# Kernel optimization log

Hardware: AMD Instinct MI355X
Metric: run time of the kernel (lower is better)

## Reference

```python
import jax, jax.numpy as jnp
import numpy as np

B, S, D = 4, 2048, 512      # batch, seq_len, input_dim
E, H = 512, 8               # embed_dim, n_heads
HD = E // H                 # head_dim
ALPHA = 1.0                 # LRSA temperature


def setup_inputs() -> dict:
    key = jax.random.key(0)
    kx, kw1, kw2 = jax.random.split(key, 3)
    # xavier_uniform bounds for the two Linear layers (bias init is 0, as in module)
    b_qkv = float(np.sqrt(6.0 / (D + 3 * E)))
    b_o = float(np.sqrt(6.0 / (E + E)))
    return {
        "x": jax.random.normal(kx, (B, S, D), dtype=jnp.float32),
        "Wqkv": jax.random.uniform(kw1, (3 * E, D), jnp.float32, -b_qkv, b_qkv),
        "bqkv": jnp.zeros((3 * E,), jnp.float32),
        "Wo": jax.random.uniform(kw2, (E, E), jnp.float32, -b_o, b_o),
        "bo": jnp.zeros((E,), jnp.float32),
    }


def reference(x, Wqkv, bqkv, Wo, bo):
    Bx, Sx, _ = x.shape
    # QKV projection: [B,S,3E] -> [B,S,H,3*HD] -> [B,H,S,3*HD]
    qkv = (x @ Wqkv.T + bqkv).reshape(Bx, Sx, H, 3 * HD).transpose(0, 2, 1, 3)
    q, k, v = jnp.split(qkv, 3, axis=-1)  # each [B,H,S,HD]

    # LRSA: pairwise squared L2 distance logits ||q_i - k_j||^2
    q_norm2 = jnp.sum(q * q, axis=-1, keepdims=True)        # [B,H,S,1]
    k_norm2 = jnp.sum(k * k, axis=-1)[..., None, :]         # [B,H,1,S]
    qk = jnp.einsum("bhqd,bhkd->bhqk", q, k)                # [B,H,S,S]
    logits = q_norm2 - 2.0 * qk + k_norm2

    # global normalizers: frobenius norm of q, max per-token L2 norm of x
    fro_q = jnp.sqrt(jnp.sum(q * q))
    inf_2_x = jnp.max(jnp.sqrt(jnp.sum(x * x, axis=-1)))
    logits = logits / fro_q / inf_2_x

    attention = jax.nn.softmax(-ALPHA * logits, axis=-1)    # [B,H,S,S]
    values = jnp.einsum("bhqk,bhkd->bhqd", attention, v)    # [B,H,S,HD]
    values = values.transpose(0, 2, 1, 3).reshape(Bx, Sx, E)
    return values @ Wo.T + bo
```

## Files before the change

kernel.cpp:

```cpp
#include <hip/hip_runtime.h>
#include <hip/hip_bf16.h>
#include <math.h>

#define B_ 4
#define S_ 2048
#define D_ 512
#define E_ 512
#define H_ 8
#define HD_ 64
#define ALPHA_ 1.0f
#define M_ (B_*S_)
#define LOG2E_ 1.44269504088896340736f

typedef __attribute__((ext_vector_type(8))) short bf16x8;
typedef __attribute__((ext_vector_type(4))) float f32x4;
typedef __attribute__((ext_vector_type(16))) float f32x16;

__device__ inline unsigned short f2bf(float f) {
    union { __hip_bfloat16 h; unsigned short u; } cv;
    cv.h = __float2bfloat16(f);
    return cv.u;
}
__device__ inline unsigned pack2bf(float a, float b) {
    union { __hip_bfloat162 h; unsigned u; } cv;
    cv.h = __float22bfloat162_rn(make_float2(a, b));
    return cv.u;
}
__device__ inline void gload16(const void* g, void* l) {
    __builtin_amdgcn_global_load_lds(
        (const __attribute__((address_space(1))) unsigned int*)g,
        (__attribute__((address_space(3))) unsigned int*)l, 16, 0, 0);
}
__device__ inline void gload4(const void* g, void* l) {
    __builtin_amdgcn_global_load_lds(
        (const __attribute__((address_space(1))) unsigned int*)g,
        (__attribute__((address_space(3))) unsigned int*)l, 4, 0, 0);
}

__global__ __launch_bounds__(256) void prep(const float* __restrict__ x,
                                            const float* __restrict__ Wqkv,
                                            const float* __restrict__ Wo,
                                            unsigned short* __restrict__ xbf,
                                            unsigned short* __restrict__ Wqkvb,
                                            unsigned short* __restrict__ Wob,
                                            float* __restrict__ xmax) {
    const int t   = threadIdx.x;
    const int bid = blockIdx.x;
    if (bid < 2048) {
        __shared__ float red[4];
        const int wid = t >> 6, lane = t & 63;
        const int row = bid * 4 + wid;
        const float* xr = &x[(size_t)row * D_ + lane * 8];
        const float4 a = *(const float4*)xr;
        const float4 b = *(const float4*)(xr + 4);
        float ss = a.x*a.x + a.y*a.y + a.z*a.z + a.w*a.w
                 + b.x*b.x + b.y*b.y + b.z*b.z + b.w*b.w;
        uint4 o;
        o.x = pack2bf(a.x, a.y); o.y = pack2bf(a.z, a.w);
        o.z = pack2bf(b.x, b.y); o.w = pack2bf(b.z, b.w);
        *(uint4*)&xbf[(size_t)row * D_ + lane * 8] = o;
        #pragma unroll
        for (int off = 32; off; off >>= 1) ss += __shfl_xor(ss, off);
        if (lane == 0) red[wid] = ss;
        __syncthreads();
        if (t == 0)
            xmax[bid] = fmaxf(fmaxf(red[0], red[1]), fmaxf(red[2], red[3]));
    } else {
        const int i  = (bid - 2048) * 256 + t;
        const int nq = 3 * E_ * D_ / 8;
        const float* src; unsigned short* dst; int j;
        if (i < nq) { src = Wqkv; dst = Wqkvb; j = i; }
        else        { src = Wo;   dst = Wob;   j = i - nq; }
        const float4 a = *(const float4*)&src[(size_t)j * 8];
        const float4 b = *(const float4*)&src[(size_t)j * 8 + 4];
        uint4 o;
        o.x = pack2bf(a.x, a.y); o.y = pack2bf(a.z, a.w);
        o.z = pack2bf(b.x, b.y); o.w = pack2bf(b.z, b.w);
        *(uint4*)&dst[(size_t)j * 8] = o;
    }
}

template<int N, int MODE>
__global__ __launch_bounds__(256) void gemm_mfma(const unsigned short* __restrict__ Abf,
                                                 const unsigned short* __restrict__ Wbf,
                                                 const float* __restrict__ bias,
                                                 void* __restrict__ out0,
                                                 void* __restrict__ out1,
                                                 void* __restrict__ out2,
                                                 float* __restrict__ part,
                                                 float* __restrict__ kn2) {
    __shared__ __align__(16) char At[16384];
    __shared__ __align__(16) char Wt[16384];

    const int t  = threadIdx.x;
    const int w  = t >> 6;
    const int l  = t & 63;
    const int g  = l >> 4;
    const int c  = l & 15;
    const int wm = w >> 1;
    const int wn = w & 1;
    const int m0 = blockIdx.y * 128;
    const int n0 = blockIdx.x * 128;

    f32x4 acc[4][4];
    #pragma unroll
    for (int i = 0; i < 4; ++i)
        #pragma unroll
        for (int j = 0; j < 4; ++j)
            #pragma unroll
            for (int r = 0; r < 4; ++r) acc[i][j][r] = 0.f;

    const int lr3 = l >> 3;
    const int colSwz = ((l & 7) * 16) ^ (lr3 << 4);
    const char* pA = (const char*)Abf + (size_t)(m0 + w * 8 + lr3) * 1024 + colSwz;
    const char* pB = (const char*)Wbf + (size_t)(n0 + w * 8 + lr3) * 1024 + colSwz;
    char* lA = At + w * 1024;
    char* lB = Wt + w * 1024;

    for (int k0 = 0; k0 < 512; k0 += 64) {
        __syncthreads();
        #pragma unroll
        for (int j = 0; j < 4; ++j) {
            gload16(pA + (size_t)j * 32768 + k0 * 2, lA + j * 4096);
            gload16(pB + (size_t)j * 32768 + k0 * 2, lB + j * 4096);
        }
        __syncthreads();

        bf16x8 af[4][2], wf[4][2];
        #pragma unroll
        for (int mt = 0; mt < 4; ++mt) {
            const int row = wm * 64 + mt * 16 + c;
            const int sw  = (row & 7) << 4;
            #pragma unroll
            for (int kc = 0; kc < 2; ++kc)
                af[mt][kc] = *(const bf16x8*)(At + row * 128 + (((kc * 4 + g) * 16) ^ sw));
        }
        #pragma unroll
        for (int nt = 0; nt < 4; ++nt) {
            const int row = wn * 64 + nt * 16 + c;
            const int sw  = (row & 7) << 4;
            #pragma unroll
            for (int kc = 0; kc < 2; ++kc)
                wf[nt][kc] = *(const bf16x8*)(Wt + row * 128 + (((kc * 4 + g) * 16) ^ sw));
        }
        #pragma unroll
        for (int mt = 0; mt < 4; ++mt)
            #pragma unroll
            for (int nt = 0; nt < 4; ++nt) {
                acc[mt][nt] = __builtin_amdgcn_mfma_f32_16x16x32_bf16(af[mt][0], wf[nt][0], acc[mt][nt], 0, 0, 0);
                acc[mt][nt] = __builtin_amdgcn_mfma_f32_16x16x32_bf16(af[mt][1], wf[nt][1], acc[mt][nt], 0, 0, 0);
            }
    }

    if (MODE == 1) {
        #pragma unroll
        for (int mt = 0; mt < 4; ++mt)
            #pragma unroll
            for (int reg = 0; reg < 4; ++reg) {
                const int m = m0 + wm * 64 + mt * 16 + g * 4 + reg;
                #pragma unroll
                for (int nt = 0; nt < 4; ++nt) {
                    const int n = n0 + wn * 64 + nt * 16 + c;
                    ((float*)out0)[(size_t)m * N + n] = acc[mt][nt][reg] + bias[n];
                }
            }
        return;
    }

    const int hb  = 2 * blockIdx.x + wn;
    const int cls = hb % 3;
    const int h   = hb / 3;
    const int b   = m0 >> 11;
    const int s0w = (m0 & 2047) + wm * 64;
    const size_t bhS = ((size_t)b * H_ + h) * S_;

    float kp[4][4];
    #pragma unroll
    for (int i = 0; i < 4; ++i)
        #pragma unroll
        for (int j = 0; j < 4; ++j) kp[i][j] = 0.f;

    if (cls == 2) {
        unsigned short* Vt_ = (unsigned short*)out2;
        #pragma unroll
        for (int nt = 0; nt < 4; ++nt) {
            const int n = n0 + wn * 64 + nt * 16 + c;
            const float bv = bias[n];
            const int d = nt * 16 + c;
            unsigned short* dbase = Vt_ + (((size_t)b * H_ + h) * HD_ + d) * S_ + s0w;
            #pragma unroll
            for (int mt = 0; mt < 4; ++mt) {
                uint2 pk;
                pk.x = pack2bf(acc[mt][nt][0] + bv, acc[mt][nt][1] + bv);
                pk.y = pack2bf(acc[mt][nt][2] + bv, acc[mt][nt][3] + bv);
                *(uint2*)&dbase[mt * 16 + g * 4] = pk;
            }
        }
    } else {
        unsigned short* dst0 = (cls == 0) ? (unsigned short*)out0 : (unsigned short*)out1;
        #pragma unroll
        for (int nt = 0; nt < 4; ++nt) {
            const int n = n0 + wn * 64 + nt * 16 + c;
            const float bv = bias[n];
            const int d = nt * 16 + c;
            #pragma unroll
            for (int mt = 0; mt < 4; ++mt)
                #pragma unroll
                for (int reg = 0; reg < 4; ++reg) {
                    const int s = s0w + mt * 16 + g * 4 + reg;
                    const float val = acc[mt][nt][reg] + bv;
                    kp[mt][reg] = fmaf(val, val, kp[mt][reg]);
                    dst0[(bhS + s) * HD_ + d] = f2bf(val);
                }
        }
    }

    __syncthreads();
    if (cls == 1) {
        float* scratch = (float*)At + wm * 1088;
        #pragma unroll
        for (int i = 0; i < 16; ++i) scratch[l * 17 + i] = kp[i >> 2][i & 3];
        asm volatile("s_waitcnt lgkmcnt(0)" ::: "memory");
        __builtin_amdgcn_sched_barrier(0);
        float sum = 0.f;
        #pragma unroll
        for (int cc = 0; cc < 16; ++cc)
            sum += scratch[(g * 16 + cc) * 17 + c];
        const int s = s0w + (c >> 2) * 16 + g * 4 + (c & 3);
        kn2[bhS + s] = sum;
    }
    __syncthreads();

    float qss = 0.f;
    if (cls == 0) {
        #pragma unroll
        for (int i = 0; i < 4; ++i)
            #pragma unroll
            for (int j = 0; j < 4; ++j) qss += kp[i][j];
    }
    float* red = (float*)At;
    red[t] = qss;
    __syncthreads();
    for (int s = 128; s; s >>= 1) {
        if (t < s) red[t] += red[t + s];
        __syncthreads();
    }
    if (t == 0) part[blockIdx.y * gridDim.x + blockIdx.x] = red[0];
}

__global__ __launch_bounds__(256) void finalize_scale(const float* __restrict__ part,
                                                      const float* __restrict__ xmax,
                                                      float* __restrict__ scal) {
    __shared__ float rs[256], rm[256];
    const int t = threadIdx.x;
    float ss = 0.f, mx = 0.f;
    for (int i = t; i < 768; i += 256) ss += part[i];
    for (int i = t; i < 2048; i += 256) mx = fmaxf(mx, xmax[i]);
    rs[t] = ss; rm[t] = mx;
    __syncthreads();
    for (int s = 128; s; s >>= 1) {
        if (t < s) { rs[t] += rs[t + s]; rm[t] = fmaxf(rm[t], rm[t + s]); }
        __syncthreads();
    }
    if (t == 0) scal[0] = ALPHA_ * LOG2E_ / (sqrtf(rs[0]) * sqrtf(rm[0]));
}

__global__ __launch_bounds__(256, 2) void attn_mfma(const unsigned short* __restrict__ Qb,
                                                    const unsigned short* __restrict__ Kb,
                                                    const unsigned short* __restrict__ Vtb,
                                                    const float* __restrict__ KN2,
                                                    const float* __restrict__ scal,
                                                    unsigned short* __restrict__ VALS) {
    __shared__ __align__(16) char lds[33280];
    char* Kl  = lds;
    char* Vl  = lds + 16384;
    char* knl = lds + 32768;

    const int t   = threadIdx.x;
    const int w   = t >> 6;
    const int l   = t & 63;
    const int h   = l >> 5;
    const int c32 = l & 31;
    const int bid  = blockIdx.y * gridDim.x + blockIdx.x;
    const int swid = (bid & 7) * 64 + (bid >> 3);
    const int bh = swid >> 4;
    const int qb = swid & 15;
    const float sc    = scal[0];
    const float ts2   = 2.0f * sc;
    const float nscal = -sc;

    const int qrow = qb * 128 + w * 32 + c32;
    const size_t qoff = ((size_t)bh * S_ + qrow) * HD_;
    bf16x8 qf[4];
    #pragma unroll
    for (int dc = 0; dc < 4; ++dc)
        qf[dc] = *(const bf16x8*)&Qb[qoff + dc * 16 + h * 8];

    f32x16 oacc0, oacc1;
    #pragma unroll
    for (int i = 0; i < 16; ++i) { oacc0[i] = 0.f; oacc1[i] = 0.f; }
    float lpart = 0.f;

    const float* kn2g = &KN2[(size_t)bh * S_];

    const int swz = (l & 7) << 4;
    int offF[2][4];
    #pragma unroll
    for (int a = 0; a < 2; ++a)
        #pragma unroll
        for (int x = 0; x < 4; ++x)
            offF[a][x] = (a * 32 + c32) * 128 + ((x * 32 + h * 16) ^ swz);

    const int lr3 = l >> 3;
    const int colSwz = ((l & 7) * 16) ^ (lr3 << 4);
    const char* pK = (const char*)Kb + ((size_t)bh * S_ * HD_) * 2
                   + (size_t)(w * 16 + lr3) * 128 + colSwz;
    const char* pV = (const char*)Vtb + ((size_t)bh * HD_ * S_) * 2
                   + (size_t)(w * 16 + lr3) * (S_ * 2) + colSwz;
    char* lK = Kl + w * 2048;
    char* lV = Vl + w * 2048;

#define STAGE(T, buf) do {                                                    \
        gload16(pK + (size_t)(T) * 8192,        lK + (buf) * 8192);           \
        gload16(pK + (size_t)(T) * 8192 + 1024, lK + (buf) * 8192 + 1024);    \
        gload16(pV + (size_t)(T) * 128,                   lV + (buf) * 8192); \
        gload16(pV + (size_t)(T) * 128 + (size_t)8 * S_ * 2,                  \
                lV + (buf) * 8192 + 1024);                                    \
        if (w == 0) gload4(kn2g + (T) * 64 + l, knl + (buf) * 256);           \
    } while (0)

    auto compute_tile = [&](int cur) {
        const char* Kc = Kl + cur * 8192;
        const char* Vc = Vl + cur * 8192;
        const float* knc = (const float*)(knl + cur * 256);

        unsigned ownw[8][2];
        #pragma unroll
        for (int st = 0; st < 2; ++st) {
            f32x16 sacc;
            #pragma unroll
            for (int i = 0; i < 16; ++i) sacc[i] = 0.f;
            #pragma unroll
            for (int dc = 0; dc < 4; ++dc) {
                const bf16x8 ka = *(const bf16x8*)(Kc + offF[st][dc]);
                sacc = __builtin_amdgcn_mfma_f32_32x32x16_bf16(ka, qf[dc], sacc, 0, 0, 0);
            }
            #pragma unroll
            for (int r4 = 0; r4 < 4; ++r4) {
                const f32x4 kn4 = *(const f32x4*)&knc[st * 32 + 8 * r4 + 4 * h];
                float pv[4];
                #pragma unroll
                for (int m = 0; m < 4; ++m) {
                    const float sl = fmaf(sacc[4 * r4 + m], ts2, nscal * kn4[m]);
                    pv[m] = exp2f(sl);
                    lpart += pv[m];
                }
                ownw[st * 4 + r4][0] = pack2bf(pv[0], pv[1]);
                ownw[st * 4 + r4][1] = pack2bf(pv[2], pv[3]);
            }
        }

        unsigned rcv[4][2];
        #pragma unroll
        for (int s = 0; s < 4; ++s) {
            const unsigned s0 = h ? ownw[2 * s][0] : ownw[2 * s + 1][0];
            const unsigned s1 = h ? ownw[2 * s][1] : ownw[2 * s + 1][1];
            rcv[s][0] = __shfl_xor(s0, 32);
            rcv[s][1] = __shfl_xor(s1, 32);
        }

        #pragma unroll
        for (int kc = 0; kc < 4; ++kc) {
            union { bf16x8 v; unsigned u[4]; } fr;
            fr.u[0] = h ? rcv[kc][0] : ownw[2 * kc][0];
            fr.u[1] = h ? rcv[kc][1] : ownw[2 * kc][1];
            fr.u[2] = h ? ownw[2 * kc + 1][0] : rcv[kc][0];
            fr.u[3] = h ? ownw[2 * kc + 1][1] : rcv[kc][1];
            const bf16x8 vb0 = *(const bf16x8*)(Vc + offF[0][kc]);
            const bf16x8 vb1 = *(const bf16x8*)(Vc + offF[1][kc]);
            oacc0 = __builtin_amdgcn_mfma_f32_32x32x16_bf16(fr.v, vb0, oacc0, 0, 0, 0);
            oacc1 = __builtin_amdgcn_mfma_f32_32x32x16_bf16(fr.v, vb1, oacc1, 0, 0, 0);
        }
    };

    STAGE(0, 0);
    __syncthreads();
    for (int T = 0; T < 32; ++T) {
        const int cur = T & 1;
        if (T < 31) STAGE(T + 1, cur ^ 1);
        compute_tile(cur);
        __syncthreads();
    }
#undef STAGE

    lpart += __shfl_xor(lpart, 32);

    const int b = bh >> 3, head = bh & 7;
    #pragma unroll
    for (int reg = 0; reg < 16; ++reg) {
        const int q_local = (reg & 3) + 8 * (reg >> 2) + 4 * h;
        const float lq  = __shfl(lpart, q_local);
        const float inv = 1.0f / lq;
        const int s = qb * 128 + w * 32 + q_local;
        unsigned short* dst = &VALS[((size_t)b * S_ + s) * E_ + head * HD_];
        dst[c32]      = f2bf(oacc0[reg] * inv);
        dst[32 + c32] = f2bf(oacc1[reg] * inv);
    }
}

extern "C" void kernel_launch(void* const* d_in, const int* in_sizes, int n_in,
                              void* d_out, int out_size, void* d_ws, size_t ws_size,
                              hipStream_t stream) {
    const float* x    = (const float*)d_in[0];
    const float* Wqkv = (const float*)d_in[1];
    const float* bqkv = (const float*)d_in[2];
    const float* Wo   = (const float*)d_in[3];
    const float* bo   = (const float*)d_in[4];
    float* out = (float*)d_out;

    char* ws = (char*)d_ws;
    unsigned short* Qb    = (unsigned short*)(ws);
    unsigned short* Kb    = (unsigned short*)(ws + ((size_t) 8 << 20));
    unsigned short* Vtb   = (unsigned short*)(ws + ((size_t)16 << 20));
    unsigned short* VALb  = (unsigned short*)(ws + ((size_t)24 << 20));
    unsigned short* xbf   = (unsigned short*)(ws + ((size_t)32 << 20));
    unsigned short* Wqkvb = (unsigned short*)(ws + ((size_t)40 << 20));
    unsigned short* Wob   = (unsigned short*)(ws + ((size_t)42 << 20));
    float* KN2  = (float*)(ws + ((size_t)43 << 20));
    float* PART = (float*)(ws + ((size_t)43 << 20) + (256 << 10));
    float* XMAX = (float*)(ws + ((size_t)43 << 20) + (260 << 10));
    float* SCAL = (float*)(ws + ((size_t)43 << 20) + (272 << 10));

    prep<<<2560, 256, 0, stream>>>(x, Wqkv, Wo, xbf, Wqkvb, Wob, XMAX);

    gemm_mfma<3 * E_, 0><<<dim3(12, 64), 256, 0, stream>>>(xbf, Wqkvb, bqkv, Qb, Kb, Vtb, PART, KN2);

    finalize_scale<<<1, 256, 0, stream>>>(PART, XMAX, SCAL);

    attn_mfma<<<dim3(16, 32), 256, 0, stream>>>(Qb, Kb, Vtb, KN2, SCAL, VALb);

    gemm_mfma<E_, 1><<<dim3(4, 64), 256, 0, stream>>>(VALb, Wob, bo, out, nullptr, nullptr, nullptr, nullptr);
}
```

Measured before the change: 122.6 us.

## Double-buffer GEMM tiles, split attention keys across wave groups, fold scale reduction

The GEMM kernel now double-buffers its LDS tiles so the next K-slice loads while MFMAs run on the current one, and raises wave priority around the MFMA block. The attention kernel moves to 512 threads, with two wave groups each handling half the key tiles and their partial outputs combined through LDS at the end. The separate finalize_scale launch is removed; each attention block recomputes the global scale from the partial sums. The half-wave bf16 exchange now uses v_permlane32_swap instead of shuffles. These changes add LDS use (about 66 KB per attention block) and repeat the scale reduction in every block, and the launch_bounds(512,4) setting may constrain register use.

```diff
diff --git a/kernel.cpp b/kernel.cpp
--- a/kernel.cpp
+++ b/kernel.cpp
@@ -89,8 +89,8 @@
                                                  void* __restrict__ out2,
                                                  float* __restrict__ part,
                                                  float* __restrict__ kn2) {
-    __shared__ __align__(16) char At[16384];
-    __shared__ __align__(16) char Wt[16384];
+    __shared__ __align__(16) char At[2][16384];
+    __shared__ __align__(16) char Wt[2][16384];
 
     const int t  = threadIdx.x;
     const int w  = t >> 6;
@@ -114,17 +114,20 @@
     const int colSwz = ((l & 7) * 16) ^ (lr3 << 4);
     const char* pA = (const char*)Abf + (size_t)(m0 + w * 8 + lr3) * 1024 + colSwz;
     const char* pB = (const char*)Wbf + (size_t)(n0 + w * 8 + lr3) * 1024 + colSwz;
-    char* lA = At + w * 1024;
-    char* lB = Wt + w * 1024;
-
-    for (int k0 = 0; k0 < 512; k0 += 64) {
-        __syncthreads();
+
+    auto gstage = [&](int k0, int buf) {
         #pragma unroll
         for (int j = 0; j < 4; ++j) {
-            gload16(pA + (size_t)j * 32768 + k0 * 2, lA + j * 4096);
-            gload16(pB + (size_t)j * 32768 + k0 * 2, lB + j * 4096);
-        }
-        __syncthreads();
+            gload16(pA + (size_t)j * 32768 + (size_t)k0 * 2, At[buf] + w * 1024 + j * 4096);
+            gload16(pB + (size_t)j * 32768 + (size_t)k0 * 2, Wt[buf] + w * 1024 + j * 4096);
+        }
+    };
+
+    gstage(0, 0);
+    __syncthreads();
+    for (int i = 0; i < 8; ++i) {
+        const int buf = i & 1;
+        if (i < 7) gstage((i + 1) * 64, buf ^ 1);
 
         bf16x8 af[4][2], wf[4][2];
         #pragma unroll
@@ -133,7 +136,7 @@
             const int sw  = (row & 7) << 4;
             #pragma unroll
             for (int kc = 0; kc < 2; ++kc)
-                af[mt][kc] = *(const bf16x8*)(At + row * 128 + (((kc * 4 + g) * 16) ^ sw));
+                af[mt][kc] = *(const bf16x8*)(At[buf] + row * 128 + (((kc * 4 + g) * 16) ^ sw));
         }
         #pragma unroll
         for (int nt = 0; nt < 4; ++nt) {
@@ -141,8 +144,9 @@
             const int sw  = (row & 7) << 4;
             #pragma unroll
             for (int kc = 0; kc < 2; ++kc)
-                wf[nt][kc] = *(const bf16x8*)(Wt + row * 128 + (((kc * 4 + g) * 16) ^ sw));
-        }
+                wf[nt][kc] = *(const bf16x8*)(Wt[buf] + row * 128 + (((kc * 4 + g) * 16) ^ sw));
+        }
+        __builtin_amdgcn_s_setprio(1);
         #pragma unroll
         for (int mt = 0; mt < 4; ++mt)
             #pragma unroll
@@ -150,6 +154,8 @@
                 acc[mt][nt] = __builtin_amdgcn_mfma_f32_16x16x32_bf16(af[mt][0], wf[nt][0], acc[mt][nt], 0, 0, 0);
                 acc[mt][nt] = __builtin_amdgcn_mfma_f32_16x16x32_bf16(af[mt][1], wf[nt][1], acc[mt][nt], 0, 0, 0);
             }
+        __builtin_amdgcn_s_setprio(0);
+        __syncthreads();
     }
 
     if (MODE == 1) {
@@ -217,7 +223,7 @@
 
     __syncthreads();
     if (cls == 1) {
-        float* scratch = (float*)At + wm * 1088;
+        float* scratch = (float*)&At[0][0] + wm * 1088;
         #pragma unroll
         for (int i = 0; i < 16; ++i) scratch[l * 17 + i] = kp[i >> 2][i & 3];
         asm volatile("s_waitcnt lgkmcnt(0)" ::: "memory");
@@ -238,7 +244,7 @@
             #pragma unroll
             for (int j = 0; j < 4; ++j) qss += kp[i][j];
     }
-    float* red = (float*)At;
+    float* red = (float*)&At[0][0];
     red[t] = qss;
     __syncthreads();
     for (int s = 128; s; s >>= 1) {
@@ -248,48 +254,49 @@
     if (t == 0) part[blockIdx.y * gridDim.x + blockIdx.x] = red[0];
 }
 
-__global__ __launch_bounds__(256) void finalize_scale(const float* __restrict__ part,
-                                                      const float* __restrict__ xmax,
-                                                      float* __restrict__ scal) {
-    __shared__ float rs[256], rm[256];
-    const int t = threadIdx.x;
-    float ss = 0.f, mx = 0.f;
-    for (int i = t; i < 768; i += 256) ss += part[i];
-    for (int i = t; i < 2048; i += 256) mx = fmaxf(mx, xmax[i]);
-    rs[t] = ss; rm[t] = mx;
-    __syncthreads();
-    for (int s = 128; s; s >>= 1) {
-        if (t < s) { rs[t] += rs[t + s]; rm[t] = fmaxf(rm[t], rm[t + s]); }
-        __syncthreads();
-    }
-    if (t == 0) scal[0] = ALPHA_ * LOG2E_ / (sqrtf(rs[0]) * sqrtf(rm[0]));
-}
-
-__global__ __launch_bounds__(256, 2) void attn_mfma(const unsigned short* __restrict__ Qb,
+__global__ __launch_bounds__(512, 4) void attn_mfma(const unsigned short* __restrict__ Qb,
                                                     const unsigned short* __restrict__ Kb,
                                                     const unsigned short* __restrict__ Vtb,
                                                     const float* __restrict__ KN2,
-                                                    const float* __restrict__ scal,
+                                                    const float* __restrict__ part,
+                                                    const float* __restrict__ xmax,
                                                     unsigned short* __restrict__ VALS) {
-    __shared__ __align__(16) char lds[33280];
-    char* Kl  = lds;
-    char* Vl  = lds + 16384;
-    char* knl = lds + 32768;
+    __shared__ __align__(16) char lds[66624];
 
     const int t   = threadIdx.x;
     const int w   = t >> 6;
     const int l   = t & 63;
     const int h   = l >> 5;
     const int c32 = l & 31;
+    const int G   = w >> 2;
+    const int wg  = w & 3;
     const int bid  = blockIdx.y * gridDim.x + blockIdx.x;
     const int swid = (bid & 7) * 64 + (bid >> 3);
     const int bh = swid >> 4;
     const int qb = swid & 15;
-    const float sc    = scal[0];
+
+    float ss = 0.f, mx = 0.f;
+    for (int i = t; i < 768; i += 512) ss += part[i];
+    for (int i = t; i < 2048; i += 512) mx = fmaxf(mx, xmax[i]);
+    #pragma unroll
+    for (int off = 32; off; off >>= 1) {
+        ss += __shfl_xor(ss, off);
+        mx = fmaxf(mx, __shfl_xor(mx, off));
+    }
+    {
+        float* red = (float*)(lds + 66560);
+        if (l == 0) { red[w] = ss; red[8 + w] = mx; }
+        __syncthreads();
+        float tss = 0.f, tmx = 0.f;
+        #pragma unroll
+        for (int i = 0; i < 8; ++i) { tss += red[i]; tmx = fmaxf(tmx, red[8 + i]); }
+        ss = tss; mx = tmx;
+    }
+    const float sc    = ALPHA_ * LOG2E_ / (sqrtf(ss) * sqrtf(mx));
     const float ts2   = 2.0f * sc;
     const float nscal = -sc;
 
-    const int qrow = qb * 128 + w * 32 + c32;
+    const int qrow = qb * 128 + wg * 32 + c32;
     const size_t qoff = ((size_t)bh * S_ + qrow) * HD_;
     bf16x8 qf[4];
     #pragma unroll
@@ -301,6 +308,9 @@
     for (int i = 0; i < 16; ++i) { oacc0[i] = 0.f; oacc1[i] = 0.f; }
     float lpart = 0.f;
 
+    char* KgB = lds + G * 32768;
+    char* VgB = KgB + 16384;
+    char* knB = lds + 65536 + G * 512;
     const float* kn2g = &KN2[(size_t)bh * S_];
 
     const int swz = (l & 7) << 4;
@@ -314,25 +324,23 @@
     const int lr3 = l >> 3;
     const int colSwz = ((l & 7) * 16) ^ (lr3 << 4);
     const char* pK = (const char*)Kb + ((size_t)bh * S_ * HD_) * 2
-                   + (size_t)(w * 16 + lr3) * 128 + colSwz;
+                   + (size_t)(wg * 16 + lr3) * 128 + colSwz;
     const char* pV = (const char*)Vtb + ((size_t)bh * HD_ * S_) * 2
-                   + (size_t)(w * 16 + lr3) * (S_ * 2) + colSwz;
-    char* lK = Kl + w * 2048;
-    char* lV = Vl + w * 2048;
+                   + (size_t)(wg * 16 + lr3) * (S_ * 2) + colSwz;
 
 #define STAGE(T, buf) do {                                                    \
-        gload16(pK + (size_t)(T) * 8192,        lK + (buf) * 8192);           \
-        gload16(pK + (size_t)(T) * 8192 + 1024, lK + (buf) * 8192 + 1024);    \
-        gload16(pV + (size_t)(T) * 128,                   lV + (buf) * 8192); \
-        gload16(pV + (size_t)(T) * 128 + (size_t)8 * S_ * 2,                  \
-                lV + (buf) * 8192 + 1024);                                    \
-        if (w == 0) gload4(kn2g + (T) * 64 + l, knl + (buf) * 256);           \
+        gload16(pK + (size_t)(T) * 8192,        KgB + (buf) * 8192 + wg * 2048);        \
+        gload16(pK + (size_t)(T) * 8192 + 1024, KgB + (buf) * 8192 + wg * 2048 + 1024); \
+        gload16(pV + (size_t)(T) * 128,         VgB + (buf) * 8192 + wg * 2048);        \
+        gload16(pV + (size_t)(T) * 128 + (size_t)8 * S_ * 2,                            \
+                VgB + (buf) * 8192 + wg * 2048 + 1024);                                 \
+        if (wg == 0) gload4(kn2g + (T) * 64 + l, knB + (buf) * 256);                    \
     } while (0)
 
     auto compute_tile = [&](int cur) {
-        const char* Kc = Kl + cur * 8192;
-        const char* Vc = Vl + cur * 8192;
-        const float* knc = (const float*)(knl + cur * 256);
+        const char* Kc = KgB + cur * 8192;
+        const char* Vc = VgB + cur * 8192;
+        const float* knc = (const float*)(knB + cur * 256);
 
         unsigned ownw[8][2];
         #pragma unroll
@@ -360,22 +368,14 @@
             }
         }
 
-        unsigned rcv[4][2];
-        #pragma unroll
-        for (int s = 0; s < 4; ++s) {
-            const unsigned s0 = h ? ownw[2 * s][0] : ownw[2 * s + 1][0];
-            const unsigned s1 = h ? ownw[2 * s][1] : ownw[2 * s + 1][1];
-            rcv[s][0] = __shfl_xor(s0, 32);
-            rcv[s][1] = __shfl_xor(s1, 32);
-        }
-
         #pragma unroll
         for (int kc = 0; kc < 4; ++kc) {
+            unsigned e0 = ownw[2 * kc][0],     e1 = ownw[2 * kc][1];
+            unsigned o0 = ownw[2 * kc + 1][0], o1 = ownw[2 * kc + 1][1];
+            asm volatile("v_permlane32_swap_b32 %0, %1" : "+v"(e0), "+v"(o0));
+            asm volatile("v_permlane32_swap_b32 %0, %1" : "+v"(e1), "+v"(o1));
             union { bf16x8 v; unsigned u[4]; } fr;
-            fr.u[0] = h ? rcv[kc][0] : ownw[2 * kc][0];
-            fr.u[1] = h ? rcv[kc][1] : ownw[2 * kc][1];
-            fr.u[2] = h ? ownw[2 * kc + 1][0] : rcv[kc][0];
-            fr.u[3] = h ? ownw[2 * kc + 1][1] : rcv[kc][1];
+            fr.u[0] = e0; fr.u[1] = e1; fr.u[2] = o0; fr.u[3] = o1;
             const bf16x8 vb0 = *(const bf16x8*)(Vc + offF[0][kc]);
             const bf16x8 vb1 = *(const bf16x8*)(Vc + offF[1][kc]);
             oacc0 = __builtin_amdgcn_mfma_f32_32x32x16_bf16(fr.v, vb0, oacc0, 0, 0, 0);
@@ -383,11 +383,11 @@
         }
     };
 
-    STAGE(0, 0);
-    __syncthreads();
-    for (int T = 0; T < 32; ++T) {
+    STAGE(G, 0);
+    __syncthreads();
+    for (int T = 0; T < 16; ++T) {
         const int cur = T & 1;
-        if (T < 31) STAGE(T + 1, cur ^ 1);
+        if (T < 15) STAGE(2 * (T + 1) + G, cur ^ 1);
         compute_tile(cur);
         __syncthreads();
     }
@@ -395,16 +395,31 @@
 
     lpart += __shfl_xor(lpart, 32);
 
-    const int b = bh >> 3, head = bh & 7;
-    #pragma unroll
-    for (int reg = 0; reg < 16; ++reg) {
-        const int q_local = (reg & 3) + 8 * (reg >> 2) + 4 * h;
-        const float lq  = __shfl(lpart, q_local);
-        const float inv = 1.0f / lq;
-        const int s = qb * 128 + w * 32 + q_local;
-        unsigned short* dst = &VALS[((size_t)b * S_ + s) * E_ + head * HD_];
-        dst[c32]      = f2bf(oacc0[reg] * inv);
-        dst[32 + c32] = f2bf(oacc1[reg] * inv);
+    float* OM = (float*)lds;
+    float* LM = (float*)(lds + 32768);
+    if (G == 1) {
+        #pragma unroll
+        for (int reg = 0; reg < 16; ++reg) {
+            const int ql = (reg & 3) + 8 * (reg >> 2) + 4 * h;
+            OM[(wg * 32 + ql) * 64 + c32]      = oacc0[reg];
+            OM[(wg * 32 + ql) * 64 + 32 + c32] = oacc1[reg];
+        }
+        if (h == 0) LM[wg * 32 + c32] = lpart;
+    }
+    __syncthreads();
+    if (G == 0) {
+        const float ltot = lpart + LM[wg * 32 + c32];
+        const int b = bh >> 3, head = bh & 7;
+        #pragma unroll
+        for (int reg = 0; reg < 16; ++reg) {
+            const int ql = (reg & 3) + 8 * (reg >> 2) + 4 * h;
+            const float lq  = __shfl(ltot, ql);
+            const float inv = 1.0f / lq;
+            const int s = qb * 128 + wg * 32 + ql;
+            unsigned short* dst = &VALS[((size_t)b * S_ + s) * E_ + head * HD_];
+            dst[c32]      = f2bf((oacc0[reg] + OM[(wg * 32 + ql) * 64 + c32]) * inv);
+            dst[32 + c32] = f2bf((oacc1[reg] + OM[(wg * 32 + ql) * 64 + 32 + c32]) * inv);
+        }
     }
 }
 
@@ -429,15 +444,12 @@
     float* KN2  = (float*)(ws + ((size_t)43 << 20));
     float* PART = (float*)(ws + ((size_t)43 << 20) + (256 << 10));
     float* XMAX = (float*)(ws + ((size_t)43 << 20) + (260 << 10));
-    float* SCAL = (float*)(ws + ((size_t)43 << 20) + (272 << 10));
 
     prep<<<2560, 256, 0, stream>>>(x, Wqkv, Wo, xbf, Wqkvb, Wob, XMAX);
 
     gemm_mfma<3 * E_, 0><<<dim3(12, 64), 256, 0, stream>>>(xbf, Wqkvb, bqkv, Qb, Kb, Vtb, PART, KN2);
 
-    finalize_scale<<<1, 256, 0, stream>>>(PART, XMAX, SCAL);
-
-    attn_mfma<<<dim3(16, 32), 256, 0, stream>>>(Qb, Kb, Vtb, KN2, SCAL, VALb);
+    attn_mfma<<<dim3(16, 32), 512, 0, stream>>>(Qb, Kb, Vtb, KN2, PART, XMAX, VALb);
 
     gemm_mfma<E_, 1><<<dim3(4, 64), 256, 0, stream>>>(VALb, Wob, bo, out, nullptr, nullptr, nullptr, nullptr);
 }
```

Result: faster. 112.7 us (-8.0%).
